# Kernel optimization log

Hardware: AMD Instinct MI355X
Metric: run time of the kernel (lower is better)

Reference implementation:

```python
import jax, jax.numpy as jnp
import numpy as np

B, S, D, H = 2, 2048, 1024, 16
DK = D // H


def setup_inputs() -> dict:
    key = jax.random.key(0)
    ks = jax.random.split(key, 6)
    scale = 1.0 / np.sqrt(D)
    return {
        "x": jax.random.normal(ks[0], (B, S, D), dtype=jnp.float32),
        "q": jax.random.normal(ks[1], (B, S, D), dtype=jnp.float32),
        "k": jax.random.normal(ks[2], (B, S, D), dtype=jnp.float32),
        "v": jax.random.normal(ks[3], (B, S, D), dtype=jnp.float32),
        "mask": jnp.ones((B, 1, S, S), dtype=jnp.int32),
        "Wq": jax.random.normal(ks[4], (D, D), dtype=jnp.float32) * scale,
        "Wo": jax.random.normal(ks[5], (D, D), dtype=jnp.float32) * scale,
    }


def reference(x, q, k, v, mask, Wq, Wo):
    b = x.shape[0]
    # NOTE: source projects q, k, v ALL through Wq (Wk/Wv unused in forward).
    def proj(t):
        # [b, s, D] -> [b, H, s, DK]   (nn.Linear: t @ W.T)
        return (t @ Wq.T).reshape(b, -1, H, DK).transpose(0, 2, 1, 3)

    query, key_, value = proj(q), proj(k), proj(v)
    # [b, H, Sq, Sk]
    scores = jnp.einsum("bhqd,bhkd->bhqk", query, key_) / np.sqrt(DK)
    scores = jnp.where(mask == 0, jnp.float32(1e-9), scores)
    attn = jax.nn.softmax(scores, axis=-1)
    out = jnp.einsum("bhqk,bhkd->bhqd", attn, value)  # [b, H, Sq, DK]
    out = out.transpose(0, 2, 1, 3).reshape(b, -1, D)
    return out @ Wo.T
```

## Files before the change

### kernel.cpp

```cpp
#include <hip/hip_runtime.h>

#define SEQ  2048
#define DDIM 1024
#define NH   16
#define DK   64

typedef _Float16 half8  __attribute__((ext_vector_type(8)));
typedef _Float16 half4v __attribute__((ext_vector_type(4)));
typedef float    floatx4 __attribute__((ext_vector_type(4)));

__device__ __forceinline__ float fast_exp2(float x) {
#if __has_builtin(__builtin_amdgcn_exp2f)
  return __builtin_amdgcn_exp2f(x);
#else
  return exp2f(x);
#endif
}

__device__ __forceinline__ half4v pack4(float e0, float e1, float e2,
                                        float e3) {
#if __has_builtin(__builtin_amdgcn_cvt_pkrtz)
  auto lo = __builtin_amdgcn_cvt_pkrtz(e0, e1);
  auto hi = __builtin_amdgcn_cvt_pkrtz(e2, e3);
  half4v p;
  *(unsigned int*)&p = __builtin_bit_cast(unsigned int, lo);
  *((unsigned int*)&p + 1) = __builtin_bit_cast(unsigned int, hi);
  return p;
#else
  half4v p;
  p[0] = (_Float16)e0; p[1] = (_Float16)e1;
  p[2] = (_Float16)e2; p[3] = (_Float16)e3;
  return p;
#endif
}

__device__ __forceinline__ void gload16(const _Float16* g, _Float16* l) {
  __builtin_amdgcn_global_load_lds(
      (const __attribute__((address_space(1))) unsigned int*)(const void*)g,
      (__attribute__((address_space(3))) unsigned int*)(void*)l, 16, 0, 0);
}

template <int NR>
__device__ __forceinline__ void stage_gl(const _Float16* __restrict__ src,
                                         int row0, int stride, int k0,
                                         _Float16* dst) {
  const int tid = threadIdx.x;
  const int w = tid >> 6, l = tid & 63;
  constexpr int RPW = NR / 4;
  const int cg = (l & 7) ^ (l >> 3);
  const _Float16* gbase = src + k0 + cg * 8;
#pragma unroll
  for (int i = 0; i < RPW / 8; ++i) {
    int rl = w * RPW + i * 8;
    gload16(gbase + (long)(row0 + rl + (l >> 3)) * stride, dst + rl * 64);
  }
}

__global__ __launch_bounds__(256) void cvt_kernel(
    const float* __restrict__ q, const float* __restrict__ k,
    const float* __restrict__ v, const float* __restrict__ Wq,
    const float* __restrict__ Wo, _Float16* __restrict__ ws) {
  long t = (long)blockIdx.x * 256 + threadIdx.x;
  long base = t * 4;
  const float* src;
  long off;
  if (base < 12582912L) {
    int which = (int)(base >> 22);
    src = which == 0 ? q : (which == 1 ? k : v);
    off = base & 4194303L;
  } else if (base < 13631488L) {
    src = Wq; off = base - 12582912L;
  } else {
    src = Wo; off = base - 13631488L;
  }
  float4 f = *(const float4*)(src + off);
  half4v h;
  h[0] = (_Float16)f.x; h[1] = (_Float16)f.y;
  h[2] = (_Float16)f.z; h[3] = (_Float16)f.w;
  *(half4v*)(ws + base) = h;
}

__device__ __forceinline__ void gemm16_gl(
    const _Float16* __restrict__ A, const _Float16* __restrict__ B,
    int m0, int n0, _Float16* As, _Float16* Bs, floatx4 (&acc)[4][4]) {
  const int tid = threadIdx.x;
  const int lane = tid & 63, w = tid >> 6;
  const int wm = w >> 1, wn = w & 1;
  const int quad = lane >> 4, l15 = lane & 15;

#pragma unroll
  for (int i = 0; i < 4; ++i)
#pragma unroll
    for (int j = 0; j < 4; ++j)
#pragma unroll
      for (int r = 0; r < 4; ++r) acc[i][j][r] = 0.f;

  stage_gl<128>(A, m0, 1024, 0, As);
  stage_gl<128>(B, n0, 1024, 0, Bs);
  __syncthreads();

  for (int kt = 0; kt < 16; ++kt) {
    _Float16* Ap = As + (kt & 1) * 8192;
    _Float16* Bp = Bs + (kt & 1) * 8192;
    if (kt < 15) {
      stage_gl<128>(A, m0, 1024, (kt + 1) * 64, As + ((kt + 1) & 1) * 8192);
      stage_gl<128>(B, n0, 1024, (kt + 1) * 64, Bs + ((kt + 1) & 1) * 8192);
    }
#pragma unroll
    for (int kc = 0; kc < 2; ++kc) {
      half8 af[4], bf[4];
#pragma unroll
      for (int i = 0; i < 4; ++i) {
        int row = wm * 64 + i * 16 + l15;
        af[i] = *(const half8*)(Ap + row * 64 + (((kc * 4 + quad) ^ (row & 7)) * 8));
      }
#pragma unroll
      for (int j = 0; j < 4; ++j) {
        int row = wn * 64 + j * 16 + l15;
        bf[j] = *(const half8*)(Bp + row * 64 + (((kc * 4 + quad) ^ (row & 7)) * 8));
      }
#pragma unroll
      for (int i = 0; i < 4; ++i)
#pragma unroll
        for (int j = 0; j < 4; ++j)
          acc[i][j] = __builtin_amdgcn_mfma_f32_16x16x32_f16(af[i], bf[j],
                                                             acc[i][j], 0, 0, 0);
    }
    __syncthreads();
  }
}

__device__ __forceinline__ void gemm16_n64_gl(
    const _Float16* __restrict__ A, const _Float16* __restrict__ B,
    int m0, int n0, _Float16* As, _Float16* Bs, floatx4 (&acc)[2][4]) {
  const int tid = threadIdx.x;
  const int lane = tid & 63, w = tid >> 6;
  const int quad = lane >> 4, l15 = lane & 15;

#pragma unroll
  for (int i = 0; i < 2; ++i)
#pragma unroll
    for (int j = 0; j < 4; ++j)
#pragma unroll
      for (int r = 0; r < 4; ++r) acc[i][j][r] = 0.f;

  stage_gl<128>(A, m0, 1024, 0, As);
  stage_gl<64>(B, n0, 1024, 0, Bs);
  __syncthreads();

  for (int kt = 0; kt < 16; ++kt) {
    _Float16* Ap = As + (kt & 1) * 8192;
    _Float16* Bp = Bs + (kt & 1) * 4096;
    if (kt < 15) {
      stage_gl<128>(A, m0, 1024, (kt + 1) * 64, As + ((kt + 1) & 1) * 8192);
      stage_gl<64>(B, n0, 1024, (kt + 1) * 64, Bs + ((kt + 1) & 1) * 4096);
    }
#pragma unroll
    for (int kc = 0; kc < 2; ++kc) {
      half8 af[2], bf[4];
#pragma unroll
      for (int i = 0; i < 2; ++i) {
        int row = w * 32 + i * 16 + l15;
        af[i] = *(const half8*)(Ap + row * 64 + (((kc * 4 + quad) ^ (row & 7)) * 8));
      }
#pragma unroll
      for (int j = 0; j < 4; ++j) {
        int row = j * 16 + l15;
        bf[j] = *(const half8*)(Bp + row * 64 + (((kc * 4 + quad) ^ (row & 7)) * 8));
      }
#pragma unroll
      for (int i = 0; i < 2; ++i)
#pragma unroll
        for (int j = 0; j < 4; ++j)
          acc[i][j] = __builtin_amdgcn_mfma_f32_16x16x32_f16(af[i], bf[j],
                                                             acc[i][j], 0, 0, 0);
    }
    __syncthreads();
  }
}

__global__ __launch_bounds__(256) void proj_gemm(
    const _Float16* __restrict__ qkv16, const _Float16* __restrict__ w16,
    _Float16* __restrict__ Qp, _Float16* __restrict__ Kp,
    _Float16* __restrict__ Vt) {
  __shared__ __align__(16) _Float16 smem[32768];
  _Float16* As = smem;
  _Float16* Bs = smem + 16384;
  const int bid = blockIdx.x;
  const int lane = threadIdx.x & 63, w = threadIdx.x >> 6;
  const int quad = lane >> 4, l15 = lane & 15;

  if (bid < 512) {
    floatx4 acc[4][4];
    const int wm = w >> 1, wn = w & 1;
    const int m0 = (bid >> 3) * 128, n0 = (bid & 7) * 128;
    gemm16_gl(qkv16, w16, m0, n0, As, Bs, acc);
#pragma unroll
    for (int i = 0; i < 4; ++i)
#pragma unroll
      for (int j = 0; j < 4; ++j)
#pragma unroll
        for (int r = 0; r < 4; ++r) {
          int m = m0 + wm * 64 + i * 16 + quad * 4 + r;
          int n = n0 + wn * 64 + j * 16 + l15;
          int seq = m & 4095;
          int b = seq >> 11, s = seq & 2047, h = n >> 6, dk = n & 63;
          long bh = b * NH + h;
          float val = acc[i][j][r];
          if (m < 4096)
            Qp[(bh * SEQ + s) * DK + dk] = (_Float16)(val * 0.180336880f);
          else
            Kp[(bh * SEQ + s) * DK + dk] = (_Float16)val;
        }
  } else {
    floatx4 acc[2][4];
    const int local = bid - 512;
    const int m0 = (local >> 6) * 128;
    const int n0 = (local & 63) * 64;
    gemm16_n64_gl(w16, qkv16 + 8388608L, m0, n0, As, Bs, acc);
#pragma unroll
    for (int i = 0; i < 2; ++i)
#pragma unroll
      for (int j = 0; j < 4; ++j)
#pragma unroll
        for (int r = 0; r < 4; ++r) {
          int m = m0 + w * 32 + i * 16 + quad * 4 + r;
          int n = n0 + j * 16 + l15;
          int h = m >> 6, dk = m & 63, b = n >> 11, s = n & 2047;
          Vt[(((long)b * NH + h) * DK + dk) * SEQ + s] = (_Float16)acc[i][j][r];
        }
  }
}

__global__ __launch_bounds__(256) void out_gemm(
    const _Float16* __restrict__ Aa, const _Float16* __restrict__ Bw,
    float* __restrict__ C) {
  __shared__ __align__(16) _Float16 smem[24576];
  _Float16* As = smem;
  _Float16* Bs = smem + 16384;
  const int bid = blockIdx.x;
  const int m0 = (bid >> 4) * 128, n0 = (bid & 15) * 64;
  floatx4 acc[2][4];
  gemm16_n64_gl(Aa, Bw, m0, n0, As, Bs, acc);

  const int lane = threadIdx.x & 63, w = threadIdx.x >> 6;
  const int quad = lane >> 4, l15 = lane & 15;
#pragma unroll
  for (int i = 0; i < 2; ++i)
#pragma unroll
    for (int j = 0; j < 4; ++j)
#pragma unroll
      for (int r = 0; r < 4; ++r) {
        int m = m0 + w * 32 + i * 16 + quad * 4 + r;
        int n = n0 + j * 16 + l15;
        C[(long)m * 1024 + n] = acc[i][j][r];
      }
}

__global__ __launch_bounds__(256) void attn_kernel(
    const _Float16* __restrict__ Qp, const _Float16* __restrict__ Kp,
    const _Float16* __restrict__ Vt, _Float16* __restrict__ Oa) {
  __shared__ __align__(16) _Float16 smem[32768];
  _Float16* Qs = smem;
  _Float16* KsB = smem + 8192;
  _Float16* VsB = smem + 16384;
  const int tid = threadIdx.x;
  const int lane = tid & 63, w = tid >> 6;
  const int quad = lane >> 4, l15 = lane & 15;
  const int c = tid & 7, r0 = tid >> 3;
  const int bh = blockIdx.y;
  const int q0 = blockIdx.x * 128;
  const _Float16* Qb = Qp + (long)bh * (SEQ * DK);
  const _Float16* Kb = Kp + (long)bh * (SEQ * DK);
  const _Float16* Vb = Vt + (long)bh * (DK * SEQ);

  half8 kreg[2], vreg[2];
  {
#pragma unroll
    for (int i = 0; i < 4; ++i) {
      int row = r0 + 32 * i;
      half8 qv = *(const half8*)(Qb + (long)(q0 + row) * DK + c * 8);
      *(half8*)(Qs + row * 64 + ((c ^ (row & 7)) * 8)) = qv;
    }
#pragma unroll
    for (int i = 0; i < 2; ++i) {
      int row = r0 + 32 * i;
      kreg[i] = *(const half8*)(Kb + (long)row * DK + c * 8);
      vreg[i] = *(const half8*)(Vb + (long)row * SEQ + c * 8);
    }
#pragma unroll
    for (int i = 0; i < 2; ++i) {
      int row = r0 + 32 * i;
      int sw = (c ^ (row & 7)) * 8;
      *(half8*)(KsB + row * 64 + sw) = kreg[i];
      *(half8*)(VsB + row * 64 + sw) = vreg[i];
    }
#pragma unroll
    for (int i = 0; i < 2; ++i) {
      int row = r0 + 32 * i;
      kreg[i] = *(const half8*)(Kb + (long)(64 + row) * DK + c * 8);
      vreg[i] = *(const half8*)(Vb + (long)row * SEQ + 64 + c * 8);
    }
  }
  __syncthreads();

  half8 qf[2][2];
#pragma unroll
  for (int qn = 0; qn < 2; ++qn)
#pragma unroll
    for (int ks = 0; ks < 2; ++ks) {
      int row = w * 32 + qn * 16 + l15;
      int cc = (ks * 4 + quad) ^ (row & 7);
      qf[qn][ks] = *(const half8*)(Qs + row * 64 + cc * 8);
    }

  floatx4 Oacc[2][4];
  float den[2] = {0.f, 0.f};
#pragma unroll
  for (int qn = 0; qn < 2; ++qn)
#pragma unroll
    for (int dt = 0; dt < 4; ++dt)
#pragma unroll
      for (int r = 0; r < 4; ++r) Oacc[qn][dt][r] = 0.f;

  half4v pbA[4][2], pbB[4][2];

  auto iter = [&](int kt, half4v (*pprev)[2], half4v (*pcur)[2]) {
    _Float16* Kcur = KsB + (kt & 1) * 4096;
    _Float16* Vprev = VsB + ((kt + 3) & 3) * 4096;
    if (kt < 31) {
      _Float16* Kwr = KsB + ((kt + 1) & 1) * 4096;
      _Float16* Vwr = VsB + ((kt + 1) & 3) * 4096;
#pragma unroll
      for (int i = 0; i < 2; ++i) {
        int row = r0 + 32 * i;
        int sw = (c ^ (row & 7)) * 8;
        *(half8*)(Kwr + row * 64 + sw) = kreg[i];
        *(half8*)(Vwr + row * 64 + sw) = vreg[i];
      }
    }
    if (kt < 30) {
      const int k0n = (kt + 2) * 64;
#pragma unroll
      for (int i = 0; i < 2; ++i) {
        int row = r0 + 32 * i;
        kreg[i] = *(const half8*)(Kb + (long)(k0n + row) * DK + c * 8);
        vreg[i] = *(const half8*)(Vb + (long)row * SEQ + k0n + c * 8);
      }
    }

#pragma unroll
    for (int mt = 0; mt < 4; ++mt) {
      floatx4 Sacc[2];
#pragma unroll
      for (int qn = 0; qn < 2; ++qn)
#pragma unroll
        for (int r = 0; r < 4; ++r) Sacc[qn][r] = 0.f;
      __builtin_amdgcn_s_setprio(1);
#pragma unroll
      for (int ks = 0; ks < 2; ++ks) {
        int row = mt * 16 + l15;
        int cc = (ks * 4 + quad) ^ (row & 7);
        half8 kf = *(const half8*)(Kcur + row * 64 + cc * 8);
#pragma unroll
        for (int qn = 0; qn < 2; ++qn)
          Sacc[qn] = __builtin_amdgcn_mfma_f32_16x16x32_f16(kf, qf[qn][ks],
                                                            Sacc[qn], 0, 0, 0);
      }
      __builtin_amdgcn_s_setprio(0);
#pragma unroll
      for (int qn = 0; qn < 2; ++qn) {
        float e0 = fast_exp2(Sacc[qn][0]);
        float e1 = fast_exp2(Sacc[qn][1]);
        float e2 = fast_exp2(Sacc[qn][2]);
        float e3 = fast_exp2(Sacc[qn][3]);
        den[qn] += (e0 + e1) + (e2 + e3);
        pcur[mt][qn] = pack4(e0, e1, e2, e3);
      }
      if (kt > 0) {
        __builtin_amdgcn_s_setprio(1);
#pragma unroll
        for (int dt = 0; dt < 4; ++dt) {
          int row = dt * 16 + l15;
          int c8 = mt * 2 + (quad >> 1);
          half4v vf = *(const half4v*)(Vprev + row * 64 +
                                       ((c8 ^ (row & 7)) * 8) + (quad & 1) * 4);
#pragma unroll
          for (int qn = 0; qn < 2; ++qn)
            Oacc[qn][dt] = __builtin_amdgcn_mfma_f32_16x16x16f16(
                vf, pprev[mt][qn], Oacc[qn][dt], 0, 0, 0);
        }
        __builtin_amdgcn_s_setprio(0);
      }
    }
    __syncthreads();
  };

  for (int kt = 0; kt < 32; kt += 2) {
    iter(kt, pbB, pbA);
    iter(kt + 1, pbA, pbB);
  }

  {
    _Float16* Vlast = VsB + 3 * 4096;
#pragma unroll
    for (int mt = 0; mt < 4; ++mt)
#pragma unroll
      for (int dt = 0; dt < 4; ++dt) {
        int row = dt * 16 + l15;
        int c8 = mt * 2 + (quad >> 1);
        half4v vf = *(const half4v*)(Vlast + row * 64 +
                                     ((c8 ^ (row & 7)) * 8) + (quad & 1) * 4);
#pragma unroll
        for (int qn = 0; qn < 2; ++qn)
          Oacc[qn][dt] = __builtin_amdgcn_mfma_f32_16x16x16f16(
              vf, pbB[mt][qn], Oacc[qn][dt], 0, 0, 0);
      }
  }

  float inv[2];
#pragma unroll
  for (int qn = 0; qn < 2; ++qn) {
    float d = den[qn];
    d += __shfl_xor(d, 16, 64);
    d += __shfl_xor(d, 32, 64);
    inv[qn] = __builtin_amdgcn_rcpf(d);
  }

#pragma unroll
  for (int qn = 0; qn < 2; ++qn)
#pragma unroll
    for (int dt = 0; dt < 4; ++dt) {
      half4v o;
#pragma unroll
      for (int r = 0; r < 4; ++r) o[r] = (_Float16)(Oacc[qn][dt][r] * inv[qn]);
      int ql = w * 32 + qn * 16 + l15;
      int c8 = dt * 2 + (quad >> 1);
      *(half4v*)(Qs + ql * 64 + ((c8 ^ (ql & 7)) * 8) + (quad & 1) * 4) = o;
    }
  __syncthreads();
  const int b = bh >> 4, h = bh & 15;
  const int qloc = tid >> 1, hf = tid & 1;
#pragma unroll
  for (int cc = 0; cc < 4; ++cc) {
    int c8 = hf * 4 + cc;
    half8 val = *(const half8*)(Qs + qloc * 64 + ((c8 ^ (qloc & 7)) * 8));
    *(half8*)(Oa + ((long)b * SEQ + q0 + qloc) * DDIM + h * DK + c8 * 8) = val;
  }
}

extern "C" void kernel_launch(void* const* d_in, const int* in_sizes, int n_in,
                              void* d_out, int out_size, void* d_ws,
                              size_t ws_size, hipStream_t stream) {
  const float* q  = (const float*)d_in[1];
  const float* k  = (const float*)d_in[2];
  const float* v  = (const float*)d_in[3];
  const float* Wq = (const float*)d_in[5];
  const float* Wo = (const float*)d_in[6];
  float* out = (float*)d_out;

  _Float16* ws     = (_Float16*)d_ws;
  _Float16* qkv16  = ws;
  _Float16* wq16   = ws + 12582912;
  _Float16* wo16   = ws + 13631488;
  _Float16* Qp     = ws + 14680064;
  _Float16* Kp     = ws + 18874368;
  _Float16* Vt     = ws + 23068672;
  _Float16* attn16 = ws + 27262976;

  cvt_kernel<<<14336, 256, 0, stream>>>(q, k, v, Wq, Wo, ws);
  proj_gemm<<<1024, 256, 0, stream>>>(qkv16, wq16, Qp, Kp, Vt);
  attn_kernel<<<dim3(16, 32), 256, 0, stream>>>(Qp, Kp, Vt, attn16);
  out_gemm<<<512, 256, 0, stream>>>(attn16, wo16, out);
}
```

Measured before the change: 237.1 us.

## Use 128x128 GEMM tiles everywhere and direct global-to-LDS staging in attention

Removes the 128x64 GEMM variant. The V-projection part of proj_gemm and the whole of out_gemm now use the 128x128 tile path, which cuts block counts to 768 and 256 and raises per-block operand reuse. The attention kernel replaces its register-prefetch-then-LDS-store pipeline for Q/K/V with the stage_gl direct global-to-LDS loads already used by the GEMMs. The larger tiles leave fewer blocks to fill the GPU (256 for out_gemm). The attention prefetch now loads only one tile ahead instead of holding a second tile in registers.

```diff
diff --git a/kernel.cpp b/kernel.cpp
--- a/kernel.cpp
+++ b/kernel.cpp
@@ -130,55 +130,6 @@
   }
 }
 
-__device__ __forceinline__ void gemm16_n64_gl(
-    const _Float16* __restrict__ A, const _Float16* __restrict__ B,
-    int m0, int n0, _Float16* As, _Float16* Bs, floatx4 (&acc)[2][4]) {
-  const int tid = threadIdx.x;
-  const int lane = tid & 63, w = tid >> 6;
-  const int quad = lane >> 4, l15 = lane & 15;
-
-#pragma unroll
-  for (int i = 0; i < 2; ++i)
-#pragma unroll
-    for (int j = 0; j < 4; ++j)
-#pragma unroll
-      for (int r = 0; r < 4; ++r) acc[i][j][r] = 0.f;
-
-  stage_gl<128>(A, m0, 1024, 0, As);
-  stage_gl<64>(B, n0, 1024, 0, Bs);
-  __syncthreads();
-
-  for (int kt = 0; kt < 16; ++kt) {
-    _Float16* Ap = As + (kt & 1) * 8192;
-    _Float16* Bp = Bs + (kt & 1) * 4096;
-    if (kt < 15) {
-      stage_gl<128>(A, m0, 1024, (kt + 1) * 64, As + ((kt + 1) & 1) * 8192);
-      stage_gl<64>(B, n0, 1024, (kt + 1) * 64, Bs + ((kt + 1) & 1) * 4096);
-    }
-#pragma unroll
-    for (int kc = 0; kc < 2; ++kc) {
-      half8 af[2], bf[4];
-#pragma unroll
-      for (int i = 0; i < 2; ++i) {
-        int row = w * 32 + i * 16 + l15;
-        af[i] = *(const half8*)(Ap + row * 64 + (((kc * 4 + quad) ^ (row & 7)) * 8));
-      }
-#pragma unroll
-      for (int j = 0; j < 4; ++j) {
-        int row = j * 16 + l15;
-        bf[j] = *(const half8*)(Bp + row * 64 + (((kc * 4 + quad) ^ (row & 7)) * 8));
-      }
-#pragma unroll
-      for (int i = 0; i < 2; ++i)
-#pragma unroll
-        for (int j = 0; j < 4; ++j)
-          acc[i][j] = __builtin_amdgcn_mfma_f32_16x16x32_f16(af[i], bf[j],
-                                                             acc[i][j], 0, 0, 0);
-    }
-    __syncthreads();
-  }
-}
-
 __global__ __launch_bounds__(256) void proj_gemm(
     const _Float16* __restrict__ qkv16, const _Float16* __restrict__ w16,
     _Float16* __restrict__ Qp, _Float16* __restrict__ Kp,
@@ -188,11 +139,11 @@
   _Float16* Bs = smem + 16384;
   const int bid = blockIdx.x;
   const int lane = threadIdx.x & 63, w = threadIdx.x >> 6;
+  const int wm = w >> 1, wn = w & 1;
   const int quad = lane >> 4, l15 = lane & 15;
+  floatx4 acc[4][4];
 
   if (bid < 512) {
-    floatx4 acc[4][4];
-    const int wm = w >> 1, wn = w & 1;
     const int m0 = (bid >> 3) * 128, n0 = (bid & 7) * 128;
     gemm16_gl(qkv16, w16, m0, n0, As, Bs, acc);
 #pragma unroll
@@ -213,19 +164,18 @@
             Kp[(bh * SEQ + s) * DK + dk] = (_Float16)val;
         }
   } else {
-    floatx4 acc[2][4];
     const int local = bid - 512;
-    const int m0 = (local >> 6) * 128;
-    const int n0 = (local & 63) * 64;
-    gemm16_n64_gl(w16, qkv16 + 8388608L, m0, n0, As, Bs, acc);
-#pragma unroll
-    for (int i = 0; i < 2; ++i)
+    const int m0 = (local >> 5) * 128;
+    const int n0 = (local & 31) * 128;
+    gemm16_gl(w16, qkv16 + 8388608L, m0, n0, As, Bs, acc);
+#pragma unroll
+    for (int i = 0; i < 4; ++i)
 #pragma unroll
       for (int j = 0; j < 4; ++j)
 #pragma unroll
         for (int r = 0; r < 4; ++r) {
-          int m = m0 + w * 32 + i * 16 + quad * 4 + r;
-          int n = n0 + j * 16 + l15;
+          int m = m0 + wm * 64 + i * 16 + quad * 4 + r;
+          int n = n0 + wn * 64 + j * 16 + l15;
           int h = m >> 6, dk = m & 63, b = n >> 11, s = n & 2047;
           Vt[(((long)b * NH + h) * DK + dk) * SEQ + s] = (_Float16)acc[i][j][r];
         }
@@ -235,24 +185,25 @@
 __global__ __launch_bounds__(256) void out_gemm(
     const _Float16* __restrict__ Aa, const _Float16* __restrict__ Bw,
     float* __restrict__ C) {
-  __shared__ __align__(16) _Float16 smem[24576];
+  __shared__ __align__(16) _Float16 smem[32768];
   _Float16* As = smem;
   _Float16* Bs = smem + 16384;
   const int bid = blockIdx.x;
-  const int m0 = (bid >> 4) * 128, n0 = (bid & 15) * 64;
-  floatx4 acc[2][4];
-  gemm16_n64_gl(Aa, Bw, m0, n0, As, Bs, acc);
+  const int m0 = (bid >> 3) * 128, n0 = (bid & 7) * 128;
+  floatx4 acc[4][4];
+  gemm16_gl(Aa, Bw, m0, n0, As, Bs, acc);
 
   const int lane = threadIdx.x & 63, w = threadIdx.x >> 6;
+  const int wm = w >> 1, wn = w & 1;
   const int quad = lane >> 4, l15 = lane & 15;
 #pragma unroll
-  for (int i = 0; i < 2; ++i)
+  for (int i = 0; i < 4; ++i)
 #pragma unroll
     for (int j = 0; j < 4; ++j)
 #pragma unroll
       for (int r = 0; r < 4; ++r) {
-        int m = m0 + w * 32 + i * 16 + quad * 4 + r;
-        int n = n0 + j * 16 + l15;
+        int m = m0 + wm * 64 + i * 16 + quad * 4 + r;
+        int n = n0 + wn * 64 + j * 16 + l15;
         C[(long)m * 1024 + n] = acc[i][j][r];
       }
 }
@@ -267,41 +218,15 @@
   const int tid = threadIdx.x;
   const int lane = tid & 63, w = tid >> 6;
   const int quad = lane >> 4, l15 = lane & 15;
-  const int c = tid & 7, r0 = tid >> 3;
   const int bh = blockIdx.y;
   const int q0 = blockIdx.x * 128;
   const _Float16* Qb = Qp + (long)bh * (SEQ * DK);
   const _Float16* Kb = Kp + (long)bh * (SEQ * DK);
   const _Float16* Vb = Vt + (long)bh * (DK * SEQ);
 
-  half8 kreg[2], vreg[2];
-  {
-#pragma unroll
-    for (int i = 0; i < 4; ++i) {
-      int row = r0 + 32 * i;
-      half8 qv = *(const half8*)(Qb + (long)(q0 + row) * DK + c * 8);
-      *(half8*)(Qs + row * 64 + ((c ^ (row & 7)) * 8)) = qv;
-    }
-#pragma unroll
-    for (int i = 0; i < 2; ++i) {
-      int row = r0 + 32 * i;
-      kreg[i] = *(const half8*)(Kb + (long)row * DK + c * 8);
-      vreg[i] = *(const half8*)(Vb + (long)row * SEQ + c * 8);
-    }
-#pragma unroll
-    for (int i = 0; i < 2; ++i) {
-      int row = r0 + 32 * i;
-      int sw = (c ^ (row & 7)) * 8;
-      *(half8*)(KsB + row * 64 + sw) = kreg[i];
-      *(half8*)(VsB + row * 64 + sw) = vreg[i];
-    }
-#pragma unroll
-    for (int i = 0; i < 2; ++i) {
-      int row = r0 + 32 * i;
-      kreg[i] = *(const half8*)(Kb + (long)(64 + row) * DK + c * 8);
-      vreg[i] = *(const half8*)(Vb + (long)row * SEQ + 64 + c * 8);
-    }
-  }
+  stage_gl<128>(Qb, q0, DK, 0, Qs);
+  stage_gl<64>(Kb, 0, DK, 0, KsB);
+  stage_gl<64>(Vb, 0, SEQ, 0, VsB);
   __syncthreads();
 
   half8 qf[2][2];
@@ -329,24 +254,8 @@
     _Float16* Kcur = KsB + (kt & 1) * 4096;
     _Float16* Vprev = VsB + ((kt + 3) & 3) * 4096;
     if (kt < 31) {
-      _Float16* Kwr = KsB + ((kt + 1) & 1) * 4096;
-      _Float16* Vwr = VsB + ((kt + 1) & 3) * 4096;
-#pragma unroll
-      for (int i = 0; i < 2; ++i) {
-        int row = r0 + 32 * i;
-        int sw = (c ^ (row & 7)) * 8;
-        *(half8*)(Kwr + row * 64 + sw) = kreg[i];
-        *(half8*)(Vwr + row * 64 + sw) = vreg[i];
-      }
-    }
-    if (kt < 30) {
-      const int k0n = (kt + 2) * 64;
-#pragma unroll
-      for (int i = 0; i < 2; ++i) {
-        int row = r0 + 32 * i;
-        kreg[i] = *(const half8*)(Kb + (long)(k0n + row) * DK + c * 8);
-        vreg[i] = *(const half8*)(Vb + (long)row * SEQ + k0n + c * 8);
-      }
+      stage_gl<64>(Kb, (kt + 1) * 64, DK, 0, KsB + ((kt + 1) & 1) * 4096);
+      stage_gl<64>(Vb, 0, SEQ, (kt + 1) * 64, VsB + ((kt + 1) & 3) * 4096);
     }
 
 #pragma unroll
@@ -469,7 +378,7 @@
   _Float16* attn16 = ws + 27262976;
 
   cvt_kernel<<<14336, 256, 0, stream>>>(q, k, v, Wq, Wo, ws);
-  proj_gemm<<<1024, 256, 0, stream>>>(qkv16, wq16, Qp, Kp, Vt);
+  proj_gemm<<<768, 256, 0, stream>>>(qkv16, wq16, Qp, Kp, Vt);
   attn_kernel<<<dim3(16, 32), 256, 0, stream>>>(Qp, Kp, Vt, attn16);
-  out_gemm<<<512, 256, 0, stream>>>(attn16, wo16, out);
-}
+  out_gemm<<<256, 256, 0, stream>>>(attn16, wo16, out);
+}
```

New measurement: 236.4 us. Within noise of the previous version (-0.3%).
